# Performance work log

Hardware: AMD Instinct MI355X
Metric: run time of the kernel (lower is better)

The kernel has to match this reference:

```python
import jax, jax.numpy as jnp
import numpy as np

N = 50000
E = 1600000
D_IN = 128
HID = 128
EPS = 1e-5
NEG_SLOPE = 0.2


def setup_inputs() -> dict:
    key = jax.random.key(0)
    ks = jax.random.split(key, 16)
    s = 1.0 / np.sqrt(D_IN)
    inp = {
        'x': jax.random.normal(ks[0], (N, D_IN), dtype=jnp.float32),
        'edge_index': jax.random.randint(ks[1], (2, E), 0, N, dtype=jnp.int64),
        # layer 0 params
        'W0': jax.random.normal(ks[2], (D_IN, HID), dtype=jnp.float32) * s,
        'att_src0': jax.random.normal(ks[3], (HID,), dtype=jnp.float32) * s,
        'att_dst0': jax.random.normal(ks[4], (HID,), dtype=jnp.float32) * s,
        'bias0': jnp.zeros((HID,), dtype=jnp.float32),
        'gamma0': jnp.ones((HID,), dtype=jnp.float32),
        'beta0': jnp.zeros((HID,), dtype=jnp.float32),
        # layer 1 params
        'W1': jax.random.normal(ks[5], (HID, HID), dtype=jnp.float32) * s,
        'att_src1': jax.random.normal(ks[6], (HID,), dtype=jnp.float32) * s,
        'att_dst1': jax.random.normal(ks[7], (HID,), dtype=jnp.float32) * s,
        'bias1': jnp.zeros((HID,), dtype=jnp.float32),
        'gamma1': jnp.ones((HID,), dtype=jnp.float32),
        'beta1': jnp.zeros((HID,), dtype=jnp.float32),
    }
    return inp


def _gat_conv(x, W, a_src, a_dst, bias, src, dst, n_nodes):
    h = x @ W                                   # [N, HID]
    alpha_src = h @ a_src                       # [N]
    alpha_dst = h @ a_dst                       # [N]
    e = jax.nn.leaky_relu(alpha_src[src] + alpha_dst[dst], NEG_SLOPE)  # [E']
    # numerically stable softmax over edges grouped by destination node
    m = jax.ops.segment_max(e, dst, num_segments=n_nodes)
    ex = jnp.exp(e - m[dst])
    denom = jax.ops.segment_sum(ex, dst, num_segments=n_nodes)
    alpha = ex / denom[dst]                     # [E']
    out = jax.ops.segment_sum(h[src] * alpha[:, None], dst, num_segments=n_nodes)
    return out + bias


def _batch_norm(x, gamma, beta):
    mean = jnp.mean(x, axis=0)
    var = jnp.mean(jnp.square(x - mean), axis=0)  # biased variance (torch BN normalization)
    return gamma * (x - mean) * jax.lax.rsqrt(var + EPS) + beta


def reference(x, edge_index, W0, att_src0, att_dst0, bias0, gamma0, beta0,
              W1, att_src1, att_dst1, bias1, gamma1, beta1):
    n = x.shape[0]
    loops = jnp.arange(n, dtype=edge_index.dtype)
    src = jnp.concatenate([edge_index[0], loops])
    dst = jnp.concatenate([edge_index[1], loops])

    h = _gat_conv(x, W0, att_src0, att_dst0, bias0, src, dst, n)
    h = _batch_norm(h, gamma0, beta0)
    h = jax.nn.relu(h)
    # dropout: identity in eval mode

    h = _gat_conv(h, W1, att_src1, att_dst1, bias1, src, dst, n)
    h = _batch_norm(h, gamma1, beta1)
    h = jax.nn.relu(h)  # last_activation=True
    return h
```

## Files before the change

kernel.cpp:

```cpp
#include <hip/hip_runtime.h>
#include <math.h>

#define HID 128
#define PAD 96
#define NB 196
#define CAP 10240
#define CHUNK 4096
#define AGG_BLOCKS 2048
#define NEG_SLOPE 0.2f
#define EPS 1e-5f

typedef __attribute__((ext_vector_type(8))) short short8;
typedef __attribute__((ext_vector_type(4))) float floatx4;

static __device__ __forceinline__ unsigned bf16_rne(float x) {
    unsigned u = __float_as_uint(x);
    return (u + 0x7fffu + ((u >> 16) & 1u)) >> 16;
}
static __device__ __forceinline__ float bf16lo_f(unsigned u) { return __uint_as_float(u << 16); }
static __device__ __forceinline__ float bf16hi_f(unsigned u) { return __uint_as_float(u & 0xffff0000u); }

__global__ void wt_build(const float* __restrict__ W, unsigned short* __restrict__ Wt) {
    int t = threadIdx.x;
    for (int task = t; task < 2048; task += 256) {
        int c = task & 127, k0 = (task >> 7) * 8;
        unsigned v[8];
#pragma unroll
        for (int j = 0; j < 8; ++j) v[j] = bf16_rne(W[(k0 + j) * HID + c]);
        uint4 st;
        st.x = v[0] | (v[1] << 16);
        st.y = v[2] | (v[3] << 16);
        st.z = v[4] | (v[5] << 16);
        st.w = v[6] | (v[7] << 16);
        *(uint4*)&Wt[c * HID + k0] = st;
    }
}

template <bool BN>
__global__ __launch_bounds__(256) void gemm_mfma(
    const float* __restrict__ X, const unsigned short* __restrict__ Wt,
    const float* __restrict__ a_src, const float* __restrict__ a_dst,
    const float* __restrict__ coef,
    unsigned short* __restrict__ Hb, float* __restrict__ asrc, float* __restrict__ adst,
    int N)
{
    int tid = threadIdx.x;
    int wv = tid >> 6, lane = tid & 63;
    int g = lane >> 4, c = lane & 15;
    int r0w = blockIdx.x * 64 + wv * 16;
    int arow = r0w + c;
    bool avalid = arow < N;
    const float* xr = X + (size_t)(avalid ? arow : 0) * HID;

    floatx4 acc[8];
#pragma unroll
    for (int i = 0; i < 8; ++i) acc[i] = (floatx4)0.f;

#pragma unroll
    for (int kc = 0; kc < 4; ++kc) {
        int k0 = kc * 32 + g * 8;
        float xv[8];
        float4 x0 = *(const float4*)&xr[k0];
        float4 x1 = *(const float4*)&xr[k0 + 4];
        xv[0] = x0.x; xv[1] = x0.y; xv[2] = x0.z; xv[3] = x0.w;
        xv[4] = x1.x; xv[5] = x1.y; xv[6] = x1.z; xv[7] = x1.w;
        if (BN) {
            float4 s0 = *(const float4*)&coef[k0];
            float4 s1 = *(const float4*)&coef[k0 + 4];
            float4 h0 = *(const float4*)&coef[HID + k0];
            float4 h1 = *(const float4*)&coef[HID + k0 + 4];
            xv[0] = fmaxf(fmaf(xv[0], s0.x, h0.x), 0.f);
            xv[1] = fmaxf(fmaf(xv[1], s0.y, h0.y), 0.f);
            xv[2] = fmaxf(fmaf(xv[2], s0.z, h0.z), 0.f);
            xv[3] = fmaxf(fmaf(xv[3], s0.w, h0.w), 0.f);
            xv[4] = fmaxf(fmaf(xv[4], s1.x, h1.x), 0.f);
            xv[5] = fmaxf(fmaf(xv[5], s1.y, h1.y), 0.f);
            xv[6] = fmaxf(fmaf(xv[6], s1.z, h1.z), 0.f);
            xv[7] = fmaxf(fmaf(xv[7], s1.w, h1.w), 0.f);
        }
        short8 af;
#pragma unroll
        for (int j = 0; j < 8; ++j) af[j] = avalid ? (short)bf16_rne(xv[j]) : (short)0;

#pragma unroll
        for (int nt = 0; nt < 8; ++nt) {
            short8 bf = *(const short8*)&Wt[(nt * 16 + c) * HID + k0];
            acc[nt] = __builtin_amdgcn_mfma_f32_16x16x32_bf16(af, bf, acc[nt], 0, 0, 0);
        }
    }

    float as_c[8], ad_c[8];
#pragma unroll
    for (int nt = 0; nt < 8; ++nt) {
        as_c[nt] = a_src[nt * 16 + c];
        ad_c[nt] = a_dst[nt * 16 + c];
    }
#pragma unroll
    for (int reg = 0; reg < 4; ++reg) {
        float s = 0.f, d = 0.f;
#pragma unroll
        for (int nt = 0; nt < 8; ++nt) {
            s = fmaf(acc[nt][reg], as_c[nt], s);
            d = fmaf(acc[nt][reg], ad_c[nt], d);
        }
#pragma unroll
        for (int o = 1; o < 16; o <<= 1) {
            s += __shfl_xor(s, o);
            d += __shfl_xor(d, o);
        }
        int crow = r0w + g * 4 + reg;
        if (c == 0 && crow < N) { asrc[crow] = s; adst[crow] = d; }
    }
#pragma unroll
    for (int reg = 0; reg < 4; ++reg) {
        int crow = r0w + g * 4 + reg;
        if (crow < N) {
#pragma unroll
            for (int nt = 0; nt < 8; ++nt)
                Hb[(size_t)crow * HID + nt * 16 + c] = (unsigned short)bf16_rne(acc[nt][reg]);
        }
    }
}

__global__ __launch_bounds__(256) void scatter_part(
    const int* __restrict__ ei, int* __restrict__ bcur,
    unsigned int* __restrict__ bbuf, int E)
{
    __shared__ int lcnt[NB], gbase[NB];
    int tid = threadIdx.x;
    int i0 = blockIdx.x * CHUNK;
    int i1 = i0 + CHUNK; if (i1 > E) i1 = E;
    if (tid < NB) lcnt[tid] = 0;
    __syncthreads();
    for (int i = i0 + tid; i < i1; i += 256)
        atomicAdd(&lcnt[ei[E + i] >> 8], 1);
    __syncthreads();
    if (tid < NB) {
        gbase[tid] = atomicAdd(&bcur[tid], lcnt[tid]);
        lcnt[tid] = 0;
    }
    __syncthreads();
    for (int i = i0 + tid; i < i1; i += 256) {
        int s = ei[i], d = ei[E + i];
        int b = d >> 8;
        int off = atomicAdd(&lcnt[b], 1);
        int pos = gbase[b] + off;
        if (pos < CAP)
            bbuf[(size_t)b * CAP + pos] = ((unsigned)s << 8) | (unsigned)(d & 255);
    }
}

__global__ __launch_bounds__(256) void ell_build(
    const unsigned int* __restrict__ bbuf, const int* __restrict__ bcur,
    int* __restrict__ cnt, int* __restrict__ ell, int N)
{
    __shared__ int stage[256 * PAD];
    __shared__ int scnt[256];
    int tid = threadIdx.x;
    int b = blockIdx.x;
    int base = b << 8;
    int nodes = N - base; if (nodes > 256) nodes = 256;

    int4 z4; z4.x = z4.y = z4.z = z4.w = 0;
    for (int idx = tid * 4; idx < 256 * PAD; idx += 1024)
        *(int4*)&stage[idx] = z4;
    __syncthreads();
    for (int i = tid; i < nodes; i += 256) {
        stage[i * PAD] = base + i;
        scnt[i] = 1;
    }
    __syncthreads();

    int nb = bcur[b]; if (nb > CAP) nb = CAP;
    const unsigned int* buf = bbuf + (size_t)b * CAP;
    for (int j = tid; j < nb; j += 256) {
        unsigned int v = buf[j];
        int dl = (int)(v & 255u);
        int s = (int)(v >> 8);
        int p = atomicAdd(&scnt[dl], 1);
        if (p < PAD) stage[dl * PAD + p] = s;
    }
    __syncthreads();

    int total = nodes * PAD;
    int* dst = ell + (size_t)base * PAD;
    for (int idx = tid * 4; idx < total; idx += 1024)
        *(int4*)&dst[idx] = *(const int4*)&stage[idx];
    for (int i = tid; i < nodes; i += 256)
        cnt[base + i] = scnt[i];
}

__global__ __launch_bounds__(256) void gat_aggregate(
    const unsigned short* __restrict__ Hb, const float* __restrict__ asrc,
    const float* __restrict__ adst, const int* __restrict__ cnt,
    const int* __restrict__ ell, const float* __restrict__ bias,
    float* __restrict__ OUT, float* __restrict__ stat, int N)
{
    __shared__ float sbuf[4][HID], qbuf[4][HID];
    int tid = threadIdx.x, wv = tid >> 6, lane = tid & 63;
    int half = lane >> 5, li = lane & 31;
    int c0 = 4 * li;
    float4 b4 = *(const float4*)&bias[c0];
    float s0 = 0.f, s1 = 0.f, s2 = 0.f, s3 = 0.f;
    float q0 = 0.f, q1 = 0.f, q2 = 0.f, q3 = 0.f;

    for (int n = blockIdx.x * 8 + wv * 2 + half; n < N; n += AGG_BLOCKS * 8) {
        int deg = cnt[n]; if (deg > PAD) deg = PAD;
        const int* row = ell + (size_t)n * PAD;
        float adn = adst[n];
        float a0 = 0.f, a1 = 0.f, a2 = 0.f, a3 = 0.f, den = 0.f;

        for (int j = 0; j < deg; j += 8) {
            int4 sA = *(const int4*)&row[j];
            int4 sB = *(const int4*)&row[j + 4];
#define EDG(SI, JOFF) { int si = (SI);                                \
            float v = asrc[si] + adn;                                 \
            v = fmaxf(v, 0.f) + NEG_SLOPE * fminf(v, 0.f);            \
            float w = ((j + JOFF) < deg) ? __expf(v) : 0.f;           \
            den += w;                                                 \
            uint2 hv = *(const uint2*)&Hb[(size_t)si * HID + c0];     \
            a0 = fmaf(w, bf16lo_f(hv.x), a0);                         \
            a1 = fmaf(w, bf16hi_f(hv.x), a1);                         \
            a2 = fmaf(w, bf16lo_f(hv.y), a2);                         \
            a3 = fmaf(w, bf16hi_f(hv.y), a3); }
            EDG(sA.x, 0) EDG(sA.y, 1) EDG(sA.z, 2) EDG(sA.w, 3)
            EDG(sB.x, 4) EDG(sB.y, 5) EDG(sB.z, 6) EDG(sB.w, 7)
#undef EDG
        }
        float inv = 1.f / den;
        float4 o;
        o.x = fmaf(a0, inv, b4.x);
        o.y = fmaf(a1, inv, b4.y);
        o.z = fmaf(a2, inv, b4.z);
        o.w = fmaf(a3, inv, b4.w);
        *(float4*)&OUT[(size_t)n * HID + c0] = o;
        s0 += o.x; s1 += o.y; s2 += o.z; s3 += o.w;
        q0 = fmaf(o.x, o.x, q0); q1 = fmaf(o.y, o.y, q1);
        q2 = fmaf(o.z, o.z, q2); q3 = fmaf(o.w, o.w, q3);
    }

    s0 += __shfl_xor(s0, 32); s1 += __shfl_xor(s1, 32);
    s2 += __shfl_xor(s2, 32); s3 += __shfl_xor(s3, 32);
    q0 += __shfl_xor(q0, 32); q1 += __shfl_xor(q1, 32);
    q2 += __shfl_xor(q2, 32); q3 += __shfl_xor(q3, 32);
    if (half == 0) {
        sbuf[wv][c0] = s0; sbuf[wv][c0 + 1] = s1;
        sbuf[wv][c0 + 2] = s2; sbuf[wv][c0 + 3] = s3;
        qbuf[wv][c0] = q0; qbuf[wv][c0 + 1] = q1;
        qbuf[wv][c0 + 2] = q2; qbuf[wv][c0 + 3] = q3;
    }
    __syncthreads();
    if (tid < HID) {
        float t = sbuf[0][tid] + sbuf[1][tid] + sbuf[2][tid] + sbuf[3][tid];
        atomicAdd(&stat[tid], t);
    } else {
        int cc = tid - HID;
        float t = qbuf[0][cc] + qbuf[1][cc] + qbuf[2][cc] + qbuf[3][cc];
        atomicAdd(&stat[HID + cc], t);
    }
}

__global__ void bn_coef(const float* __restrict__ stat, const float* __restrict__ gamma,
                        const float* __restrict__ beta, float* __restrict__ coef,
                        float invN)
{
    int c = threadIdx.x;
    float mean = stat[c] * invN;
    float var = stat[HID + c] * invN - mean * mean;
    float s = gamma[c] * rsqrtf(var + EPS);
    coef[c] = s;
    coef[HID + c] = beta[c] - mean * s;
}

__global__ __launch_bounds__(256) void bn_apply(
    float* __restrict__ X, const float* __restrict__ coef, int N)
{
    int tid = threadIdx.x, lane = tid & 63, wv = tid >> 6;
    int c0 = 2 * lane;
    float s0 = coef[c0], s1 = coef[c0 + 1];
    float h0 = coef[HID + c0], h1 = coef[HID + c0 + 1];
    for (int r = blockIdx.x * 4 + wv; r < N; r += gridDim.x * 4) {
        float2 v = *(float2*)&X[(size_t)r * HID + c0];
        float y0 = fmaxf(fmaf(v.x, s0, h0), 0.f);
        float y1 = fmaxf(fmaf(v.y, s1, h1), 0.f);
        *(float2*)&X[(size_t)r * HID + c0] = make_float2(y0, y1);
    }
}

extern "C" void kernel_launch(void* const* d_in, const int* in_sizes, int n_in,
                              void* d_out, int out_size, void* d_ws, size_t ws_size,
                              hipStream_t stream)
{
    const float* x        = (const float*)d_in[0];
    const int*   ei       = (const int*)d_in[1];
    const float* W0       = (const float*)d_in[2];
    const float* att_src0 = (const float*)d_in[3];
    const float* att_dst0 = (const float*)d_in[4];
    const float* bias0    = (const float*)d_in[5];
    const float* gamma0   = (const float*)d_in[6];
    const float* beta0    = (const float*)d_in[7];
    const float* W1       = (const float*)d_in[8];
    const float* att_src1 = (const float*)d_in[9];
    const float* att_dst1 = (const float*)d_in[10];
    const float* bias1    = (const float*)d_in[11];
    const float* gamma1   = (const float*)d_in[12];
    const float* beta1    = (const float*)d_in[13];

    const int N = in_sizes[0] / HID;
    const int E = in_sizes[1] / 2;
    float* out = (float*)d_out;

    char* wsbase = (char*)d_ws;
    size_t off = 0;
    auto alloc = [&](size_t bytes) -> void* {
        void* p = wsbase + off;
        off += (bytes + 255) & ~(size_t)255;
        return p;
    };
    unsigned short* Hb   = (unsigned short*)alloc((size_t)N * HID * 2);
    float*          asrc = (float*)alloc((size_t)N * 4);
    float*          adst = (float*)alloc((size_t)N * 4);
    int*            cnt  = (int*)  alloc((size_t)N * 4);
    int*            ell  = (int*)  alloc((size_t)N * PAD * 4);
    unsigned int*   bbuf = (unsigned int*)alloc((size_t)NB * CAP * 4);
    int*            bcur = (int*)  alloc(NB * 4);
    float*          stats = (float*)alloc(4 * HID * 4);
    float*          coef0 = (float*)alloc(2 * HID * 4);
    float*          coef1 = (float*)alloc(2 * HID * 4);
    unsigned short* Wt0  = (unsigned short*)alloc(HID * HID * 2);
    unsigned short* Wt1  = (unsigned short*)alloc(HID * HID * 2);
    float* stat0 = stats;
    float* stat1 = stats + 2 * HID;

    const int gemm_blocks  = (N + 63) / 64;
    const int part_blocks  = (E + CHUNK - 1) / CHUNK;
    const int build_blocks = (N + 255) / 256;
    const float invN = 1.0f / (float)N;

    (void)hipMemsetAsync(bcur, 0, NB * 4, stream);
    (void)hipMemsetAsync(stats, 0, 4 * HID * 4, stream);

    wt_build<<<1, 256, 0, stream>>>(W0, Wt0);
    wt_build<<<1, 256, 0, stream>>>(W1, Wt1);
    scatter_part<<<part_blocks, 256, 0, stream>>>(ei, bcur, bbuf, E);
    ell_build<<<build_blocks, 256, 0, stream>>>(bbuf, bcur, cnt, ell, N);

    gemm_mfma<false><<<gemm_blocks, 256, 0, stream>>>(
        x, Wt0, att_src0, att_dst0, nullptr, Hb, asrc, adst, N);
    gat_aggregate<<<AGG_BLOCKS, 256, 0, stream>>>(
        Hb, asrc, adst, cnt, ell, bias0, out, stat0, N);
    bn_coef<<<1, HID, 0, stream>>>(stat0, gamma0, beta0, coef0, invN);

    gemm_mfma<true><<<gemm_blocks, 256, 0, stream>>>(
        out, Wt1, att_src1, att_dst1, coef0, Hb, asrc, adst, N);
    gat_aggregate<<<AGG_BLOCKS, 256, 0, stream>>>(
        Hb, asrc, adst, cnt, ell, bias1, out, stat1, N);
    bn_coef<<<1, HID, 0, stream>>>(stat1, gamma1, beta1, coef1, invN);
    bn_apply<<<2048, 256, 0, stream>>>(out, coef1, N);
}
```

Before: 338.3 us.

## Map one node per wavefront with scalar edge indices and sentinel-padded ELL rows

The aggregation kernel now gives each wavefront one destination node, with each lane handling two channels. The node index is forced wave-uniform so the ELL row and attention-score loads can go through the scalar path. Padding ELL slots now point to a sentinel node N, whose source score is -1e30 and whose bf16 feature row is zeroed. That makes the padded edges contribute zero weight, so the per-edge degree check can be dropped. The trade-off is fewer independent nodes in flight per wave, which may lower memory-level parallelism for the gathers.

```diff
diff --git a/kernel.cpp b/kernel.cpp
--- a/kernel.cpp
+++ b/kernel.cpp
@@ -20,8 +20,10 @@
 static __device__ __forceinline__ float bf16lo_f(unsigned u) { return __uint_as_float(u << 16); }
 static __device__ __forceinline__ float bf16hi_f(unsigned u) { return __uint_as_float(u & 0xffff0000u); }
 
-__global__ void wt_build(const float* __restrict__ W, unsigned short* __restrict__ Wt) {
+__global__ void wt_build(const float* __restrict__ W, unsigned short* __restrict__ Wt,
+                         unsigned short* __restrict__ Hb, int N) {
     int t = threadIdx.x;
+    if (t < 64) ((unsigned*)(Hb + (size_t)N * HID))[t] = 0u;
     for (int task = t; task < 2048; task += 256) {
         int c = task & 127, k0 = (task >> 7) * 8;
         unsigned v[8];
@@ -152,7 +154,7 @@
 
 __global__ __launch_bounds__(256) void ell_build(
     const unsigned int* __restrict__ bbuf, const int* __restrict__ bcur,
-    int* __restrict__ cnt, int* __restrict__ ell, int N)
+    int* __restrict__ cnt, int* __restrict__ ell, float* __restrict__ asrc, int N)
 {
     __shared__ int stage[256 * PAD];
     __shared__ int scnt[256];
@@ -161,9 +163,11 @@
     int base = b << 8;
     int nodes = N - base; if (nodes > 256) nodes = 256;
 
-    int4 z4; z4.x = z4.y = z4.z = z4.w = 0;
+    if (b == 0 && tid == 0) asrc[N] = -1e30f;
+
+    int4 s4; s4.x = s4.y = s4.z = s4.w = N;
     for (int idx = tid * 4; idx < 256 * PAD; idx += 1024)
-        *(int4*)&stage[idx] = z4;
+        *(int4*)&stage[idx] = s4;
     __syncthreads();
     for (int i = tid; i < nodes; i += 256) {
         stage[i * PAD] = base + i;
@@ -198,57 +202,42 @@
 {
     __shared__ float sbuf[4][HID], qbuf[4][HID];
     int tid = threadIdx.x, wv = tid >> 6, lane = tid & 63;
-    int half = lane >> 5, li = lane & 31;
-    int c0 = 4 * li;
-    float4 b4 = *(const float4*)&bias[c0];
-    float s0 = 0.f, s1 = 0.f, s2 = 0.f, s3 = 0.f;
-    float q0 = 0.f, q1 = 0.f, q2 = 0.f, q3 = 0.f;
-
-    for (int n = blockIdx.x * 8 + wv * 2 + half; n < N; n += AGG_BLOCKS * 8) {
-        int deg = cnt[n]; if (deg > PAD) deg = PAD;
-        const int* row = ell + (size_t)n * PAD;
-        float adn = adst[n];
-        float a0 = 0.f, a1 = 0.f, a2 = 0.f, a3 = 0.f, den = 0.f;
+    int c0 = 2 * lane;
+    float b0 = bias[c0], b1 = bias[c0 + 1];
+    float ssum0 = 0.f, ssum1 = 0.f, sq0 = 0.f, sq1 = 0.f;
+
+    for (int n = blockIdx.x * 4 + wv; n < N; n += AGG_BLOCKS * 4) {
+        int nn = __builtin_amdgcn_readfirstlane(n);
+        int deg = cnt[nn]; if (deg > PAD) deg = PAD;
+        const int* row = ell + (size_t)nn * PAD;
+        float adn = adst[nn];
+        float acc0 = 0.f, acc1 = 0.f, den = 0.f;
 
         for (int j = 0; j < deg; j += 8) {
             int4 sA = *(const int4*)&row[j];
             int4 sB = *(const int4*)&row[j + 4];
-#define EDG(SI, JOFF) { int si = (SI);                                \
+#define EDG(SI) { int si = (SI);                                      \
             float v = asrc[si] + adn;                                 \
-            v = fmaxf(v, 0.f) + NEG_SLOPE * fminf(v, 0.f);            \
-            float w = ((j + JOFF) < deg) ? __expf(v) : 0.f;           \
+            v = fmaxf(v, v * NEG_SLOPE);                              \
+            float w = __expf(v);                                      \
             den += w;                                                 \
-            uint2 hv = *(const uint2*)&Hb[(size_t)si * HID + c0];     \
-            a0 = fmaf(w, bf16lo_f(hv.x), a0);                         \
-            a1 = fmaf(w, bf16hi_f(hv.x), a1);                         \
-            a2 = fmaf(w, bf16lo_f(hv.y), a2);                         \
-            a3 = fmaf(w, bf16hi_f(hv.y), a3); }
-            EDG(sA.x, 0) EDG(sA.y, 1) EDG(sA.z, 2) EDG(sA.w, 3)
-            EDG(sB.x, 4) EDG(sB.y, 5) EDG(sB.z, 6) EDG(sB.w, 7)
+            unsigned hv = *(const unsigned*)(Hb + (size_t)si * HID + c0); \
+            acc0 = fmaf(w, bf16lo_f(hv), acc0);                       \
+            acc1 = fmaf(w, bf16hi_f(hv), acc1); }
+            EDG(sA.x) EDG(sA.y) EDG(sA.z) EDG(sA.w)
+            EDG(sB.x) EDG(sB.y) EDG(sB.z) EDG(sB.w)
 #undef EDG
         }
         float inv = 1.f / den;
-        float4 o;
-        o.x = fmaf(a0, inv, b4.x);
-        o.y = fmaf(a1, inv, b4.y);
-        o.z = fmaf(a2, inv, b4.z);
-        o.w = fmaf(a3, inv, b4.w);
-        *(float4*)&OUT[(size_t)n * HID + c0] = o;
-        s0 += o.x; s1 += o.y; s2 += o.z; s3 += o.w;
-        q0 = fmaf(o.x, o.x, q0); q1 = fmaf(o.y, o.y, q1);
-        q2 = fmaf(o.z, o.z, q2); q3 = fmaf(o.w, o.w, q3);
-    }
-
-    s0 += __shfl_xor(s0, 32); s1 += __shfl_xor(s1, 32);
-    s2 += __shfl_xor(s2, 32); s3 += __shfl_xor(s3, 32);
-    q0 += __shfl_xor(q0, 32); q1 += __shfl_xor(q1, 32);
-    q2 += __shfl_xor(q2, 32); q3 += __shfl_xor(q3, 32);
-    if (half == 0) {
-        sbuf[wv][c0] = s0; sbuf[wv][c0 + 1] = s1;
-        sbuf[wv][c0 + 2] = s2; sbuf[wv][c0 + 3] = s3;
-        qbuf[wv][c0] = q0; qbuf[wv][c0 + 1] = q1;
-        qbuf[wv][c0 + 2] = q2; qbuf[wv][c0 + 3] = q3;
-    }
+        float o0 = fmaf(acc0, inv, b0);
+        float o1 = fmaf(acc1, inv, b1);
+        *(float2*)&OUT[(size_t)nn * HID + c0] = make_float2(o0, o1);
+        ssum0 += o0; ssum1 += o1;
+        sq0 = fmaf(o0, o0, sq0); sq1 = fmaf(o1, o1, sq1);
+    }
+
+    sbuf[wv][c0] = ssum0; sbuf[wv][c0 + 1] = ssum1;
+    qbuf[wv][c0] = sq0;   qbuf[wv][c0 + 1] = sq1;
     __syncthreads();
     if (tid < HID) {
         float t = sbuf[0][tid] + sbuf[1][tid] + sbuf[2][tid] + sbuf[3][tid];
@@ -317,8 +306,8 @@
         off += (bytes + 255) & ~(size_t)255;
         return p;
     };
-    unsigned short* Hb   = (unsigned short*)alloc((size_t)N * HID * 2);
-    float*          asrc = (float*)alloc((size_t)N * 4);
+    unsigned short* Hb   = (unsigned short*)alloc((size_t)(N + 1) * HID * 2);
+    float*          asrc = (float*)alloc((size_t)(N + 1) * 4);
     float*          adst = (float*)alloc((size_t)N * 4);
     int*            cnt  = (int*)  alloc((size_t)N * 4);
     int*            ell  = (int*)  alloc((size_t)N * PAD * 4);
@@ -340,10 +329,10 @@
     (void)hipMemsetAsync(bcur, 0, NB * 4, stream);
     (void)hipMemsetAsync(stats, 0, 4 * HID * 4, stream);
 
-    wt_build<<<1, 256, 0, stream>>>(W0, Wt0);
-    wt_build<<<1, 256, 0, stream>>>(W1, Wt1);
+    wt_build<<<1, 256, 0, stream>>>(W0, Wt0, Hb, N);
+    wt_build<<<1, 256, 0, stream>>>(W1, Wt1, Hb, N);
     scatter_part<<<part_blocks, 256, 0, stream>>>(ei, bcur, bbuf, E);
-    ell_build<<<build_blocks, 256, 0, stream>>>(bbuf, bcur, cnt, ell, N);
+    ell_build<<<build_blocks, 256, 0, stream>>>(bbuf, bcur, cnt, ell, asrc, N);
 
     gemm_mfma<false><<<gemm_blocks, 256, 0, stream>>>(
         x, Wt0, att_src0, att_dst0, nullptr, Hb, asrc, adst, N);
```

Result: faster. 309.1 us (-8.6%).
